# Performance work log

Measured on AMD Instinct MI355X. Metric: run time of the kernel, lower is better.

## Reference

```python
import jax, jax.numpy as jnp
import numpy as np

N_NODES = 100000
N_EDGES = 800000
D_IN = 128
D_HID = 128


def setup_inputs() -> dict:
    key = jax.random.key(0)
    ks = jax.random.split(key, 5)
    x = jax.random.normal(ks[0], (N_NODES, D_IN), dtype=jnp.float32)
    edge_index = jax.random.randint(ks[1], (2, N_EDGES), 0, N_NODES, dtype=jnp.int64)
    W1 = jax.random.normal(ks[2], (D_HID, D_IN), dtype=jnp.float32) * 0.05
    b1 = jnp.zeros((D_HID,), dtype=jnp.float32)
    W2 = jax.random.normal(ks[3], (D_HID, D_HID), dtype=jnp.float32) * 0.05
    b2 = jnp.zeros((D_HID,), dtype=jnp.float32)
    return {"x": x, "edge_index": edge_index, "W1": W1, "b1": b1, "W2": W2, "b2": b2}


def _gcn_conv(x, W, b, src, dst, norm, num_nodes):
    # x' = x @ W^T, then scatter-add normalized messages to dst, then + bias
    h = x @ W.T                                  # [N, d_out]
    msg = h[src] * norm[:, None]                 # [E+N, d_out] gather + scale
    out = jax.ops.segment_sum(msg, dst, num_segments=num_nodes)
    return out + b


def reference(x, edge_index, W1, b1, W2, b2):
    n = x.shape[0]
    loops = jnp.arange(n, dtype=edge_index.dtype)
    src = jnp.concatenate([edge_index[0], loops])  # self-loops appended (PyG GCNConv)
    dst = jnp.concatenate([edge_index[1], loops])
    # symmetric normalization: deg over target nodes (weight 1 per edge)
    deg = jax.ops.segment_sum(jnp.ones_like(dst, dtype=x.dtype), dst, num_segments=n)
    dis = jnp.where(deg > 0, jax.lax.rsqrt(jnp.maximum(deg, 1e-12)), 0.0)
    norm = dis[src] * dis[dst]
    h = jax.nn.relu(_gcn_conv(x, W1, b1, src, dst, norm, n))
    return _gcn_conv(h, W2, b2, src, dst, norm, n)
```

## Files before the change

kernel.cpp:

```cpp
#include <hip/hip_runtime.h>

#define D 128
#define CAP 48
#define BE 4096
#define SC 5120

typedef __attribute__((ext_vector_type(8))) short bf16x8;
typedef __attribute__((ext_vector_type(4))) float f32x4;
typedef __attribute__((ext_vector_type(8))) unsigned short u16x8;

__device__ inline unsigned short f2bf(float f) {
    unsigned u = __float_as_uint(f);
    return (unsigned short)((u + 0x7fff + ((u >> 16) & 1)) >> 16);
}
__device__ inline float bf2f(unsigned short s) {
    return __uint_as_float((unsigned)s << 16);
}
__device__ inline bf16x8 cvt8(const float* __restrict__ p) {
    float4 a = *(const float4*)p;
    float4 b = *(const float4*)(p + 4);
    bf16x8 r;
    r[0] = (short)f2bf(a.x); r[1] = (short)f2bf(a.y);
    r[2] = (short)f2bf(a.z); r[3] = (short)f2bf(a.w);
    r[4] = (short)f2bf(b.x); r[5] = (short)f2bf(b.y);
    r[6] = (short)f2bf(b.z); r[7] = (short)f2bf(b.w);
    return r;
}

__global__ void k_prep(const float* __restrict__ W1, const float* __restrict__ W2,
                       unsigned short* __restrict__ Wb1, unsigned short* __restrict__ Wb2,
                       int* __restrict__ bcnt, int NBK) {
    int i = blockIdx.x * 256 + threadIdx.x;
    if (i < D * D) { Wb1[i] = f2bf(W1[i]); Wb2[i] = f2bf(W2[i]); }
    if (i < NBK) bcnt[i] = 0;
}


template <bool INBF16, bool FOLD>
__device__ inline void gemm_tile(const void* __restrict__ in_v,
                                 const unsigned short* __restrict__ Wb,
                                 const int* __restrict__ cnt,
                                 unsigned short* __restrict__ g,
                                 int N, int tile, int t) {
    int w = t >> 6, l = t & 63;
    int r16 = l & 15, g4 = l >> 4;
    int base = tile * 128 + w * 32;
    int row0 = base + r16, row1 = row0 + 16;
    int cr0 = (row0 < N) ? row0 : N - 1;
    int cr1 = (row1 < N) ? row1 : N - 1;

    f32x4 acc0[8] = {};
    f32x4 acc1[8] = {};
    const unsigned short* wr = Wb + r16 * D + g4 * 8;

#pragma unroll 1
    for (int ks = 0; ks < 4; ks++) {
        bf16x8 b0, b1;
        if (INBF16) {
            const unsigned short* h = (const unsigned short*)in_v;
            b0 = *(const bf16x8*)(h + (size_t)cr0 * D + g4 * 8 + ks * 32);
            b1 = *(const bf16x8*)(h + (size_t)cr1 * D + g4 * 8 + ks * 32);
        } else {
            const float* xx = (const float*)in_v;
            b0 = cvt8(xx + (size_t)cr0 * D + g4 * 8 + ks * 32);
            b1 = cvt8(xx + (size_t)cr1 * D + g4 * 8 + ks * 32);
        }
#pragma unroll
        for (int jt = 0; jt < 8; jt++) {
            bf16x8 a = *(const bf16x8*)(wr + jt * 16 * D + ks * 32);
            acc0[jt] = __builtin_amdgcn_mfma_f32_16x16x32_bf16(a, b0, acc0[jt], 0, 0, 0);
            acc1[jt] = __builtin_amdgcn_mfma_f32_16x16x32_bf16(a, b1, acc1[jt], 0, 0, 0);
        }
    }

#pragma unroll
    for (int tt = 0; tt < 2; tt++) {
        int row = base + tt * 16 + r16;
        if (row < N) {
            float dv = 1.0f;
            if (FOLD) {
                int dg = cnt[row]; if (dg > CAP) dg = CAP;
                dv = rsqrtf((float)(dg + 1));
            }
#pragma unroll
            for (int jt = 0; jt < 8; jt++) {
                f32x4 a = tt ? acc1[jt] : acc0[jt];
                ushort4 o = { f2bf(a[0] * dv), f2bf(a[1] * dv),
                              f2bf(a[2] * dv), f2bf(a[3] * dv) };
                *(ushort4*)&g[(size_t)row * D + jt * 16 + g4 * 4] = o;
            }
        }
    }
}


__global__ __launch_bounds__(256) void k_sort_gemm1(
        const int* __restrict__ ei, int* __restrict__ bcnt, unsigned* __restrict__ brec,
        const float* __restrict__ x, const unsigned short* __restrict__ Wb1,
        unsigned short* __restrict__ g, int N, int E, int ntiles, int fb, int NBK) {
    int bid = blockIdx.x;
    if (bid % 5 == 4) {
        __shared__ unsigned srt[BE];
        __shared__ unsigned char bko[BE];
        __shared__ int hist[256];
        __shared__ int pfx[256];
        __shared__ int gbase[256];
        __shared__ int cur[256];
        int f = bid / 5;
        if (f >= fb) return;
        int t = threadIdx.x;
        int e0 = f * BE;
        int n = E - e0; if (n > BE) n = BE;

        hist[t] = 0; cur[t] = 0;
        __syncthreads();

        unsigned rec[16]; int mb[16];
#pragma unroll
        for (int j = 0; j < 16; j++) {
            int e = e0 + j * 256 + t;
            if (e < E) {
                int s = ei[e], d = ei[E + e];
                rec[j] = ((unsigned)s << 9) | (unsigned)(d & 511);
                mb[j] = d >> 9;
                atomicAdd(&hist[mb[j]], 1);
            } else mb[j] = -1;
        }
        __syncthreads();
        int v = hist[t];
        pfx[t] = v;
        __syncthreads();
        for (int dd = 1; dd < 256; dd <<= 1) {
            int xv = (t >= dd) ? pfx[t - dd] : 0;
            __syncthreads();
            pfx[t] += xv;
            __syncthreads();
        }
        pfx[t] -= v;
        if (v > 0 && t < NBK) gbase[t] = atomicAdd(&bcnt[t], v);
        __syncthreads();
#pragma unroll
        for (int j = 0; j < 16; j++) {
            if (mb[j] >= 0) {
                int p = pfx[mb[j]] + atomicAdd(&cur[mb[j]], 1);
                srt[p] = rec[j];
                bko[p] = (unsigned char)mb[j];
            }
        }
        __syncthreads();
        for (int i = t; i < n; i += 256) {
            int b = bko[i];
            int pos = gbase[b] + (i - pfx[b]);
            if (pos < SC) brec[(size_t)b * SC + pos] = srt[i];
        }
    } else {
        int gid = (bid / 5) * 4 + (bid % 5);
        if (gid >= ntiles) return;
        gemm_tile<false, false>(x, Wb1, nullptr, g, N, gid, threadIdx.x);
    }
}


__global__ __launch_bounds__(256) void k_build(const int* __restrict__ bcnt,
                                               const unsigned* __restrict__ brec,
                                               int* __restrict__ cnt,
                                               int* __restrict__ col, int N) {
    __shared__ int c512[512];
    int b = blockIdx.x, t = threadIdx.x;
    c512[t] = 0; c512[t + 256] = 0;
    __syncthreads();
    int total = bcnt[b]; if (total > SC) total = SC;
    for (int i = t; i < total; i += 256) {
        unsigned rec = brec[(size_t)b * SC + i];
        int dl = rec & 511;
        int p = atomicAdd(&c512[dl], 1);
        if (p < CAP) col[(size_t)(b * 512 + dl) * CAP + p] = (int)(rec >> 9);
    }
    __syncthreads();
#pragma unroll
    for (int k = 0; k < 2; k++) {
        int dl = t + k * 256;
        int node = b * 512 + dl;
        if (node < N) cnt[node] = (c512[dl] < CAP) ? c512[dl] : CAP;
    }
}

__global__ __launch_bounds__(256) void k_gemm2(
        const unsigned short* __restrict__ h, const unsigned short* __restrict__ Wb2,
        const int* __restrict__ cnt, unsigned short* __restrict__ g, int N, int ntiles) {
    if ((int)blockIdx.x >= ntiles) return;
    gemm_tile<true, true>(h, Wb2, cnt, g, N, blockIdx.x, threadIdx.x);
}


template <bool RELU, bool OUT_BF16, bool DISU>
__global__ __launch_bounds__(256) void k_agg(const unsigned short* __restrict__ gtab,
                                             const int* __restrict__ cnt,
                                             const int* __restrict__ col,
                                             const float* __restrict__ bias,
                                             void* __restrict__ out, int N) {
    int node = blockIdx.x * 16 + (threadIdx.x >> 4);
    if (node >= N) return;
    int l16 = threadIdx.x & 15;
    const u16x8* G = (const u16x8*)gtab;
    int deg = cnt[node];
    float disv = rsqrtf((float)(deg + 1));
    float acc[8];
    {
        u16x8 s = G[(size_t)node * 16 + l16];
        float sf = DISU ? disv : 1.0f;
#pragma unroll
        for (int j = 0; j < 8; j++) acc[j] = bf2f(s[j]) * sf;
    }
    const int* cbase = col + (size_t)node * CAP;
    int i = 0;
    for (; i + 3 < deg; i += 4) {
        int u0 = cbase[i], u1 = cbase[i + 1], u2 = cbase[i + 2], u3 = cbase[i + 3];
        u16x8 m0 = G[(size_t)u0 * 16 + l16];
        u16x8 m1 = G[(size_t)u1 * 16 + l16];
        u16x8 m2 = G[(size_t)u2 * 16 + l16];
        u16x8 m3 = G[(size_t)u3 * 16 + l16];
        if (DISU) {
            float d0 = rsqrtf((float)(cnt[u0] + 1));
            float d1 = rsqrtf((float)(cnt[u1] + 1));
            float d2 = rsqrtf((float)(cnt[u2] + 1));
            float d3 = rsqrtf((float)(cnt[u3] + 1));
#pragma unroll
            for (int j = 0; j < 8; j++)
                acc[j] += (bf2f(m0[j]) * d0 + bf2f(m1[j]) * d1)
                        + (bf2f(m2[j]) * d2 + bf2f(m3[j]) * d3);
        } else {
#pragma unroll
            for (int j = 0; j < 8; j++)
                acc[j] += (bf2f(m0[j]) + bf2f(m1[j])) + (bf2f(m2[j]) + bf2f(m3[j]));
        }
    }
    for (; i < deg; i++) {
        int u = cbase[i];
        u16x8 m = G[(size_t)u * 16 + l16];
        float du = DISU ? rsqrtf((float)(cnt[u] + 1)) : 1.0f;
#pragma unroll
        for (int j = 0; j < 8; j++) acc[j] += bf2f(m[j]) * du;
    }
    const float4* B4 = (const float4*)bias;
    float4 bb0 = B4[l16 * 2], bb1 = B4[l16 * 2 + 1];
    float r[8];
    r[0] = fmaf(acc[0], disv, bb0.x); r[1] = fmaf(acc[1], disv, bb0.y);
    r[2] = fmaf(acc[2], disv, bb0.z); r[3] = fmaf(acc[3], disv, bb0.w);
    r[4] = fmaf(acc[4], disv, bb1.x); r[5] = fmaf(acc[5], disv, bb1.y);
    r[6] = fmaf(acc[6], disv, bb1.z); r[7] = fmaf(acc[7], disv, bb1.w);
    if (RELU) {
#pragma unroll
        for (int j = 0; j < 8; j++) r[j] = fmaxf(r[j], 0.f);
    }
    if (OUT_BF16) {
        u16x8 o;
#pragma unroll
        for (int j = 0; j < 8; j++) o[j] = f2bf(r[j]);
        ((u16x8*)out)[(size_t)node * 16 + l16] = o;
    } else {
        float4 o0 = make_float4(r[0], r[1], r[2], r[3]);
        float4 o1 = make_float4(r[4], r[5], r[6], r[7]);
        ((float4*)out)[(size_t)node * 32 + l16 * 2]     = o0;
        ((float4*)out)[(size_t)node * 32 + l16 * 2 + 1] = o1;
    }
}


extern "C" void kernel_launch(void* const* d_in, const int* in_sizes, int n_in,
                              void* d_out, int out_size, void* d_ws, size_t ws_size,
                              hipStream_t stream) {
    const float* x  = (const float*)d_in[0];
    const int*   ei = (const int*)d_in[1];
    const float* W1 = (const float*)d_in[2];
    const float* b1 = (const float*)d_in[3];
    const float* W2 = (const float*)d_in[4];
    const float* b2 = (const float*)d_in[5];
    float* out = (float*)d_out;

    int N = in_sizes[0] / D;
    int E = in_sizes[1] / 2;
    int NBK = (N + 511) >> 9;

    char* w = (char*)d_ws;
    unsigned short* g = (unsigned short*)w;  size_t off = (size_t)N * D * 2;
    off = (off + 255) & ~(size_t)255;
    int* cnt  = (int*)(w + off);             off += (size_t)N * 4;
    off = (off + 255) & ~(size_t)255;
    int* col  = (int*)(w + off);             off += (size_t)NBK * 512 * CAP * 4;
    off = (off + 255) & ~(size_t)255;
    unsigned short* Wb1 = (unsigned short*)(w + off); off += (size_t)D * D * 2;
    unsigned short* Wb2 = (unsigned short*)(w + off); off += (size_t)D * D * 2;
    off = (off + 255) & ~(size_t)255;
    int* bcnt = (int*)(w + off);             off += (size_t)NBK * 4;
    off = (off + 255) & ~(size_t)255;
    unsigned* brec = (unsigned*)(w + off);   off += (size_t)NBK * SC * 4;
    unsigned short* h = (unsigned short*)d_out;

    int ntiles = (N + 127) / 128;
    int fillB  = (E + BE - 1) / BE;
    int fb = fillB > (ntiles + 3) / 4 ? fillB : (ntiles + 3) / 4;
    int total  = 5 * fb;

    k_prep<<<(D * D + 255) / 256, 256, 0, stream>>>(W1, W2, Wb1, Wb2, bcnt, NBK);

    k_sort_gemm1<<<total, 256, 0, stream>>>(ei, bcnt, brec, x, Wb1, g, N, E,
                                            ntiles, fillB, NBK);
    k_build<<<NBK, 256, 0, stream>>>(bcnt, brec, cnt, col, N);

    k_agg<true, true, true><<<(N + 15) / 16, 256, 0, stream>>>(g, cnt, col, b1, h, N);

    k_gemm2<<<ntiles, 256, 0, stream>>>(h, Wb2, cnt, g, N, ntiles);

    k_agg<false, false, false><<<(N + 15) / 16, 256, 0, stream>>>(g, cnt, col, b2, out, N);
}
```

Baseline: 160.1 us.

## Fuse layer-1 aggregation with GEMM2 via LDS and switch to compact CSR

Fuses the first aggregation (with ReLU) and the second GEMM into one kernel. Each block aggregates 128 nodes into an LDS tile and then runs the MFMA GEMM from LDS, so the intermediate h is never written to or read back from global memory. The adjacency changes from fixed-CAP padded rows to an exact CSR built with a per-bucket prefix scan and a global atomic offset, which removes the degree cap and the padding. It also unrolls the gather loops by 8. The cost is an LDS-heavy fused kernel with only 782 blocks, where each 16-lane group handles 8 nodes one after another, which may hurt latency hiding. Bucket order in the CSR becomes nondeterministic.

```diff
diff --git a/kernel.cpp b/kernel.cpp
--- a/kernel.cpp
+++ b/kernel.cpp
@@ -1,9 +1,9 @@
 #include <hip/hip_runtime.h>
 
 #define D 128
-#define CAP 48
 #define BE 4096
 #define SC 5120
+#define LROW 136
 
 typedef __attribute__((ext_vector_type(8))) short bf16x8;
 typedef __attribute__((ext_vector_type(4))) float f32x4;
@@ -29,19 +29,18 @@
 
 __global__ void k_prep(const float* __restrict__ W1, const float* __restrict__ W2,
                        unsigned short* __restrict__ Wb1, unsigned short* __restrict__ Wb2,
-                       int* __restrict__ bcnt, int NBK) {
+                       int* __restrict__ bcnt, int* __restrict__ gcnt, int NBK) {
     int i = blockIdx.x * 256 + threadIdx.x;
     if (i < D * D) { Wb1[i] = f2bf(W1[i]); Wb2[i] = f2bf(W2[i]); }
     if (i < NBK) bcnt[i] = 0;
-}
-
-
-template <bool INBF16, bool FOLD>
-__device__ inline void gemm_tile(const void* __restrict__ in_v,
-                                 const unsigned short* __restrict__ Wb,
-                                 const int* __restrict__ cnt,
-                                 unsigned short* __restrict__ g,
-                                 int N, int tile, int t) {
+    if (i == D * D) *gcnt = 0;
+}
+
+
+__device__ inline void gemm_tile_f32in(const float* __restrict__ xx,
+                                       const unsigned short* __restrict__ Wb,
+                                       unsigned short* __restrict__ g,
+                                       int N, int tile, int t) {
     int w = t >> 6, l = t & 63;
     int r16 = l & 15, g4 = l >> 4;
     int base = tile * 128 + w * 32;
@@ -55,16 +54,8 @@
 
 #pragma unroll 1
     for (int ks = 0; ks < 4; ks++) {
-        bf16x8 b0, b1;
-        if (INBF16) {
-            const unsigned short* h = (const unsigned short*)in_v;
-            b0 = *(const bf16x8*)(h + (size_t)cr0 * D + g4 * 8 + ks * 32);
-            b1 = *(const bf16x8*)(h + (size_t)cr1 * D + g4 * 8 + ks * 32);
-        } else {
-            const float* xx = (const float*)in_v;
-            b0 = cvt8(xx + (size_t)cr0 * D + g4 * 8 + ks * 32);
-            b1 = cvt8(xx + (size_t)cr1 * D + g4 * 8 + ks * 32);
-        }
+        bf16x8 b0 = cvt8(xx + (size_t)cr0 * D + g4 * 8 + ks * 32);
+        bf16x8 b1 = cvt8(xx + (size_t)cr1 * D + g4 * 8 + ks * 32);
 #pragma unroll
         for (int jt = 0; jt < 8; jt++) {
             bf16x8 a = *(const bf16x8*)(wr + jt * 16 * D + ks * 32);
@@ -72,21 +63,14 @@
             acc1[jt] = __builtin_amdgcn_mfma_f32_16x16x32_bf16(a, b1, acc1[jt], 0, 0, 0);
         }
     }
-
 #pragma unroll
     for (int tt = 0; tt < 2; tt++) {
         int row = base + tt * 16 + r16;
         if (row < N) {
-            float dv = 1.0f;
-            if (FOLD) {
-                int dg = cnt[row]; if (dg > CAP) dg = CAP;
-                dv = rsqrtf((float)(dg + 1));
-            }
 #pragma unroll
             for (int jt = 0; jt < 8; jt++) {
                 f32x4 a = tt ? acc1[jt] : acc0[jt];
-                ushort4 o = { f2bf(a[0] * dv), f2bf(a[1] * dv),
-                              f2bf(a[2] * dv), f2bf(a[3] * dv) };
+                ushort4 o = { f2bf(a[0]), f2bf(a[1]), f2bf(a[2]), f2bf(a[3]) };
                 *(ushort4*)&g[(size_t)row * D + jt * 16 + g4 * 4] = o;
             }
         }
@@ -156,7 +140,7 @@
     } else {
         int gid = (bid / 5) * 4 + (bid % 5);
         if (gid >= ntiles) return;
-        gemm_tile<false, false>(x, Wb1, nullptr, g, N, gid, threadIdx.x);
+        gemm_tile_f32in(x, Wb1, g, N, gid, threadIdx.x);
     }
 }
 
@@ -164,106 +148,208 @@
 __global__ __launch_bounds__(256) void k_build(const int* __restrict__ bcnt,
                                                const unsigned* __restrict__ brec,
                                                int* __restrict__ cnt,
-                                               int* __restrict__ col, int N) {
+                                               int* __restrict__ rp,
+                                               int* __restrict__ col,
+                                               int* __restrict__ gcnt, int N) {
     __shared__ int c512[512];
+    __shared__ int base512[512];
+    __shared__ int psc[256];
+    __shared__ int bksum;
     int b = blockIdx.x, t = threadIdx.x;
     c512[t] = 0; c512[t + 256] = 0;
     __syncthreads();
     int total = bcnt[b]; if (total > SC) total = SC;
+    for (int i = t; i < total; i += 256)
+        atomicAdd(&c512[brec[(size_t)b * SC + i] & 511], 1);
+    __syncthreads();
+    int d0 = c512[2 * t], d1 = c512[2 * t + 1];
+    int pair = d0 + d1;
+    psc[t] = pair;
+    __syncthreads();
+    for (int dd = 1; dd < 256; dd <<= 1) {
+        int xv = (t >= dd) ? psc[t - dd] : 0;
+        __syncthreads();
+        psc[t] += xv;
+        __syncthreads();
+    }
+    int pexc = psc[t] - pair;
+    if (t == 255) bksum = atomicAdd(gcnt, psc[255]);
+    __syncthreads();
+    int gb = bksum;
+    base512[2 * t]     = gb + pexc;
+    base512[2 * t + 1] = gb + pexc + d0;
+    c512[2 * t] = 0; c512[2 * t + 1] = 0;
+    __syncthreads();
     for (int i = t; i < total; i += 256) {
         unsigned rec = brec[(size_t)b * SC + i];
         int dl = rec & 511;
         int p = atomicAdd(&c512[dl], 1);
-        if (p < CAP) col[(size_t)(b * 512 + dl) * CAP + p] = (int)(rec >> 9);
+        col[base512[dl] + p] = (int)(rec >> 9);
     }
     __syncthreads();
 #pragma unroll
     for (int k = 0; k < 2; k++) {
         int dl = t + k * 256;
         int node = b * 512 + dl;
-        if (node < N) cnt[node] = (c512[dl] < CAP) ? c512[dl] : CAP;
-    }
-}
-
-__global__ __launch_bounds__(256) void k_gemm2(
-        const unsigned short* __restrict__ h, const unsigned short* __restrict__ Wb2,
-        const int* __restrict__ cnt, unsigned short* __restrict__ g, int N, int ntiles) {
-    if ((int)blockIdx.x >= ntiles) return;
-    gemm_tile<true, true>(h, Wb2, cnt, g, N, blockIdx.x, threadIdx.x);
-}
-
-
-template <bool RELU, bool OUT_BF16, bool DISU>
-__global__ __launch_bounds__(256) void k_agg(const unsigned short* __restrict__ gtab,
-                                             const int* __restrict__ cnt,
-                                             const int* __restrict__ col,
-                                             const float* __restrict__ bias,
-                                             void* __restrict__ out, int N) {
+        if (node < N) { cnt[node] = c512[dl]; rp[node] = base512[dl]; }
+    }
+}
+
+
+__global__ __launch_bounds__(256) void k_agg1_gemm2(
+        const unsigned short* __restrict__ g, const int* __restrict__ cnt,
+        const int* __restrict__ rp, const int* __restrict__ col,
+        const float* __restrict__ b1, const unsigned short* __restrict__ Wb2,
+        unsigned short* __restrict__ g2, int N, int ntiles) {
+    __shared__ __align__(16) unsigned short hl[128 * LROW];
+    int tile = blockIdx.x;
+    if (tile >= ntiles) return;
+    int t = threadIdx.x, grp = t >> 4, l16 = t & 15;
+    const u16x8* G = (const u16x8*)g;
+    const float4* B4 = (const float4*)b1;
+    float4 bb0 = B4[l16 * 2], bb1 = B4[l16 * 2 + 1];
+
+#pragma unroll 1
+    for (int ii = 0; ii < 8; ii++) {
+        int local = grp * 8 + ii;
+        int node = tile * 128 + local;
+        u16x8 hv = {};
+        if (node < N) {
+            int deg = cnt[node];
+            float disv = rsqrtf((float)(deg + 1));
+            float acc[8];
+            u16x8 s = G[(size_t)node * 16 + l16];
+#pragma unroll
+            for (int j = 0; j < 8; j++) acc[j] = bf2f(s[j]) * disv;
+            const int* cb = col + rp[node];
+            int i = 0;
+            for (; i + 7 < deg; i += 8) {
+                int u[8]; u16x8 m[8]; float dd[8];
+#pragma unroll
+                for (int k = 0; k < 8; k++) u[k] = cb[i + k];
+#pragma unroll
+                for (int k = 0; k < 8; k++) m[k] = G[(size_t)u[k] * 16 + l16];
+#pragma unroll
+                for (int k = 0; k < 8; k++) dd[k] = rsqrtf((float)(cnt[u[k]] + 1));
+#pragma unroll
+                for (int j = 0; j < 8; j++) {
+                    float s0 = fmaf(bf2f(m[0][j]), dd[0], bf2f(m[1][j]) * dd[1]);
+                    float s1 = fmaf(bf2f(m[2][j]), dd[2], bf2f(m[3][j]) * dd[3]);
+                    float s2 = fmaf(bf2f(m[4][j]), dd[4], bf2f(m[5][j]) * dd[5]);
+                    float s3 = fmaf(bf2f(m[6][j]), dd[6], bf2f(m[7][j]) * dd[7]);
+                    acc[j] += (s0 + s1) + (s2 + s3);
+                }
+            }
+            for (; i < deg; i++) {
+                int u = cb[i];
+                u16x8 m = G[(size_t)u * 16 + l16];
+                float du = rsqrtf((float)(cnt[u] + 1));
+#pragma unroll
+                for (int j = 0; j < 8; j++) acc[j] += bf2f(m[j]) * du;
+            }
+            float r[8];
+            r[0] = fmaf(acc[0], disv, bb0.x); r[1] = fmaf(acc[1], disv, bb0.y);
+            r[2] = fmaf(acc[2], disv, bb0.z); r[3] = fmaf(acc[3], disv, bb0.w);
+            r[4] = fmaf(acc[4], disv, bb1.x); r[5] = fmaf(acc[5], disv, bb1.y);
+            r[6] = fmaf(acc[6], disv, bb1.z); r[7] = fmaf(acc[7], disv, bb1.w);
+#pragma unroll
+            for (int j = 0; j < 8; j++) hv[j] = f2bf(fmaxf(r[j], 0.f));
+        }
+        *(u16x8*)&hl[local * LROW + l16 * 8] = hv;
+    }
+    __syncthreads();
+
+    int w = t >> 6, l = t & 63;
+    int r16 = l & 15, g4 = l >> 4;
+    int base = tile * 128 + w * 32;
+    f32x4 acc0[8] = {};
+    f32x4 acc1[8] = {};
+    const unsigned short* wr = Wb2 + r16 * D + g4 * 8;
+    int xb0 = (w * 32 + r16) * LROW + g4 * 8;
+    int xb1 = xb0 + 16 * LROW;
+#pragma unroll 1
+    for (int ks = 0; ks < 4; ks++) {
+        bf16x8 b0 = *(const bf16x8*)&hl[xb0 + ks * 32];
+        bf16x8 b1v = *(const bf16x8*)&hl[xb1 + ks * 32];
+#pragma unroll
+        for (int jt = 0; jt < 8; jt++) {
+            bf16x8 a = *(const bf16x8*)(wr + jt * 16 * D + ks * 32);
+            acc0[jt] = __builtin_amdgcn_mfma_f32_16x16x32_bf16(a, b0, acc0[jt], 0, 0, 0);
+            acc1[jt] = __builtin_amdgcn_mfma_f32_16x16x32_bf16(a, b1v, acc1[jt], 0, 0, 0);
+        }
+    }
+#pragma unroll
+    for (int tt = 0; tt < 2; tt++) {
+        int row = base + tt * 16 + r16;
+        if (row < N) {
+            float dv = rsqrtf((float)(cnt[row] + 1));
+#pragma unroll
+            for (int jt = 0; jt < 8; jt++) {
+                f32x4 a = tt ? acc1[jt] : acc0[jt];
+                ushort4 o = { f2bf(a[0] * dv), f2bf(a[1] * dv),
+                              f2bf(a[2] * dv), f2bf(a[3] * dv) };
+                *(ushort4*)&g2[(size_t)row * D + jt * 16 + g4 * 4] = o;
+            }
+        }
+    }
+}
+
+
+__global__ __launch_bounds__(256) void k_agg2(
+        const unsigned short* __restrict__ g2, const int* __restrict__ cnt,
+        const int* __restrict__ rp, const int* __restrict__ col,
+        const float* __restrict__ b2, float* __restrict__ out, int N) {
     int node = blockIdx.x * 16 + (threadIdx.x >> 4);
     if (node >= N) return;
     int l16 = threadIdx.x & 15;
-    const u16x8* G = (const u16x8*)gtab;
-    int deg = cnt[node];
-    float disv = rsqrtf((float)(deg + 1));
+    const u16x8* G = (const u16x8*)g2;
     float acc[8];
     {
         u16x8 s = G[(size_t)node * 16 + l16];
-        float sf = DISU ? disv : 1.0f;
-#pragma unroll
-        for (int j = 0; j < 8; j++) acc[j] = bf2f(s[j]) * sf;
-    }
-    const int* cbase = col + (size_t)node * CAP;
+#pragma unroll
+        for (int j = 0; j < 8; j++) acc[j] = bf2f(s[j]);
+    }
+    int deg = cnt[node];
+    const int* cb = col + rp[node];
     int i = 0;
+    for (; i + 7 < deg; i += 8) {
+        int u[8]; u16x8 m[8];
+#pragma unroll
+        for (int k = 0; k < 8; k++) u[k] = cb[i + k];
+#pragma unroll
+        for (int k = 0; k < 8; k++) m[k] = G[(size_t)u[k] * 16 + l16];
+#pragma unroll
+        for (int j = 0; j < 8; j++) {
+            float s0 = (bf2f(m[0][j]) + bf2f(m[1][j])) + (bf2f(m[2][j]) + bf2f(m[3][j]));
+            float s1 = (bf2f(m[4][j]) + bf2f(m[5][j])) + (bf2f(m[6][j]) + bf2f(m[7][j]));
+            acc[j] += s0 + s1;
+        }
+    }
     for (; i + 3 < deg; i += 4) {
-        int u0 = cbase[i], u1 = cbase[i + 1], u2 = cbase[i + 2], u3 = cbase[i + 3];
+        int u0 = cb[i], u1 = cb[i + 1], u2 = cb[i + 2], u3 = cb[i + 3];
         u16x8 m0 = G[(size_t)u0 * 16 + l16];
         u16x8 m1 = G[(size_t)u1 * 16 + l16];
         u16x8 m2 = G[(size_t)u2 * 16 + l16];
         u16x8 m3 = G[(size_t)u3 * 16 + l16];
-        if (DISU) {
-            float d0 = rsqrtf((float)(cnt[u0] + 1));
-            float d1 = rsqrtf((float)(cnt[u1] + 1));
-            float d2 = rsqrtf((float)(cnt[u2] + 1));
-            float d3 = rsqrtf((float)(cnt[u3] + 1));
-#pragma unroll
-            for (int j = 0; j < 8; j++)
-                acc[j] += (bf2f(m0[j]) * d0 + bf2f(m1[j]) * d1)
-                        + (bf2f(m2[j]) * d2 + bf2f(m3[j]) * d3);
-        } else {
-#pragma unroll
-            for (int j = 0; j < 8; j++)
-                acc[j] += (bf2f(m0[j]) + bf2f(m1[j])) + (bf2f(m2[j]) + bf2f(m3[j]));
-        }
+#pragma unroll
+        for (int j = 0; j < 8; j++)
+            acc[j] += (bf2f(m0[j]) + bf2f(m1[j])) + (bf2f(m2[j]) + bf2f(m3[j]));
     }
     for (; i < deg; i++) {
-        int u = cbase[i];
-        u16x8 m = G[(size_t)u * 16 + l16];
-        float du = DISU ? rsqrtf((float)(cnt[u] + 1)) : 1.0f;
-#pragma unroll
-        for (int j = 0; j < 8; j++) acc[j] += bf2f(m[j]) * du;
-    }
-    const float4* B4 = (const float4*)bias;
+        u16x8 m = G[(size_t)cb[i] * 16 + l16];
+#pragma unroll
+        for (int j = 0; j < 8; j++) acc[j] += bf2f(m[j]);
+    }
+    float disv = rsqrtf((float)(deg + 1));
+    const float4* B4 = (const float4*)b2;
     float4 bb0 = B4[l16 * 2], bb1 = B4[l16 * 2 + 1];
-    float r[8];
-    r[0] = fmaf(acc[0], disv, bb0.x); r[1] = fmaf(acc[1], disv, bb0.y);
-    r[2] = fmaf(acc[2], disv, bb0.z); r[3] = fmaf(acc[3], disv, bb0.w);
-    r[4] = fmaf(acc[4], disv, bb1.x); r[5] = fmaf(acc[5], disv, bb1.y);
-    r[6] = fmaf(acc[6], disv, bb1.z); r[7] = fmaf(acc[7], disv, bb1.w);
-    if (RELU) {
-#pragma unroll
-        for (int j = 0; j < 8; j++) r[j] = fmaxf(r[j], 0.f);
-    }
-    if (OUT_BF16) {
-        u16x8 o;
-#pragma unroll
-        for (int j = 0; j < 8; j++) o[j] = f2bf(r[j]);
-        ((u16x8*)out)[(size_t)node * 16 + l16] = o;
-    } else {
-        float4 o0 = make_float4(r[0], r[1], r[2], r[3]);
-        float4 o1 = make_float4(r[4], r[5], r[6], r[7]);
-        ((float4*)out)[(size_t)node * 32 + l16 * 2]     = o0;
-        ((float4*)out)[(size_t)node * 32 + l16 * 2 + 1] = o1;
-    }
+    float4 o0, o1;
+    o0.x = fmaf(acc[0], disv, bb0.x); o0.y = fmaf(acc[1], disv, bb0.y);
+    o0.z = fmaf(acc[2], disv, bb0.z); o0.w = fmaf(acc[3], disv, bb0.w);
+    o1.x = fmaf(acc[4], disv, bb1.x); o1.y = fmaf(acc[5], disv, bb1.y);
+    o1.z = fmaf(acc[6], disv, bb1.z); o1.w = fmaf(acc[7], disv, bb1.w);
+    ((float4*)out)[(size_t)node * 32 + l16 * 2]     = o0;
+    ((float4*)out)[(size_t)node * 32 + l16 * 2 + 1] = o1;
 }
 
 
@@ -283,34 +369,36 @@
     int NBK = (N + 511) >> 9;
 
     char* w = (char*)d_ws;
-    unsigned short* g = (unsigned short*)w;  size_t off = (size_t)N * D * 2;
+    unsigned short* g  = (unsigned short*)w;  size_t off = (size_t)N * D * 2;
+    off = (off + 255) & ~(size_t)255;
+    unsigned short* g2 = (unsigned short*)(w + off); off += (size_t)N * D * 2;
     off = (off + 255) & ~(size_t)255;
     int* cnt  = (int*)(w + off);             off += (size_t)N * 4;
     off = (off + 255) & ~(size_t)255;
-    int* col  = (int*)(w + off);             off += (size_t)NBK * 512 * CAP * 4;
+    int* rp   = (int*)(w + off);             off += (size_t)N * 4;
+    off = (off + 255) & ~(size_t)255;
+    int* col  = (int*)(w + off);             off += (size_t)E * 4;
     off = (off + 255) & ~(size_t)255;
     unsigned short* Wb1 = (unsigned short*)(w + off); off += (size_t)D * D * 2;
     unsigned short* Wb2 = (unsigned short*)(w + off); off += (size_t)D * D * 2;
     off = (off + 255) & ~(size_t)255;
     int* bcnt = (int*)(w + off);             off += (size_t)NBK * 4;
     off = (off + 255) & ~(size_t)255;
+    int* gcnt = (int*)(w + off);             off += 256;
     unsigned* brec = (unsigned*)(w + off);   off += (size_t)NBK * SC * 4;
-    unsigned short* h = (unsigned short*)d_out;
 
     int ntiles = (N + 127) / 128;
     int fillB  = (E + BE - 1) / BE;
     int fb = fillB > (ntiles + 3) / 4 ? fillB : (ntiles + 3) / 4;
     int total  = 5 * fb;
 
-    k_prep<<<(D * D + 255) / 256, 256, 0, stream>>>(W1, W2, Wb1, Wb2, bcnt, NBK);
+    k_prep<<<(D * D + 511) / 256, 256, 0, stream>>>(W1, W2, Wb1, Wb2, bcnt, gcnt, NBK);
 
     k_sort_gemm1<<<total, 256, 0, stream>>>(ei, bcnt, brec, x, Wb1, g, N, E,
                                             ntiles, fillB, NBK);
-    k_build<<<NBK, 256, 0, stream>>>(bcnt, brec, cnt, col, N);
-
-    k_agg<true, true, true><<<(N + 15) / 16, 256, 0, stream>>>(g, cnt, col, b1, h, N);
-
-    k_gemm2<<<ntiles, 256, 0, stream>>>(h, Wb2, cnt, g, N, ntiles);
-
-    k_agg<false, false, false><<<(N + 15) / 16, 256, 0, stream>>>(g, cnt, col, b2, out, N);
-}
+    k_build<<<NBK, 256, 0, stream>>>(bcnt, brec, cnt, rp, col, gcnt, N);
+
+    k_agg1_gemm2<<<ntiles, 256, 0, stream>>>(g, cnt, rp, col, b1, Wb2, g2, N, ntiles);
+
+    k_agg2<<<(N + 15) / 16, 256, 0, stream>>>(g2, cnt, rp, col, b2, out, N);
+}
```

Measured after the change: 207.8 us. 1.3x slower.

## Replace fixed-capacity adjacency with compact CSR and aggregate two nodes per group

Applied to the files above, without the earlier changes.

Replaces the padded per-node adjacency (capacity 48 slots) with a compact CSR layout: k_build histograms destinations, prefix-sums them, and reserves a global offset per bucket through an atomic counter, then writes columns contiguously. The degree cap is removed, which changes semantics for very high-degree nodes and moves it closer to the reference. Each aggregation thread group now handles two nodes, with masked loads that keep more gathers in flight. A separate g2 buffer is used for the second GEMM output. The CSR build adds a scan and a second pass over the records, and the padded lanes in aggregation issue redundant loads of node n0 (with weight zero) whenever the two degrees differ.

```diff
diff --git a/kernel.cpp b/kernel.cpp
--- a/kernel.cpp
+++ b/kernel.cpp
@@ -1,7 +1,6 @@
 #include <hip/hip_runtime.h>
 
 #define D 128
-#define CAP 48
 #define BE 4096
 #define SC 5120
 
@@ -29,10 +28,11 @@
 
 __global__ void k_prep(const float* __restrict__ W1, const float* __restrict__ W2,
                        unsigned short* __restrict__ Wb1, unsigned short* __restrict__ Wb2,
-                       int* __restrict__ bcnt, int NBK) {
+                       int* __restrict__ bcnt, int* __restrict__ gcnt, int NBK) {
     int i = blockIdx.x * 256 + threadIdx.x;
     if (i < D * D) { Wb1[i] = f2bf(W1[i]); Wb2[i] = f2bf(W2[i]); }
     if (i < NBK) bcnt[i] = 0;
+    if (i == D * D) *gcnt = 0;
 }
 
 
@@ -72,16 +72,12 @@
             acc1[jt] = __builtin_amdgcn_mfma_f32_16x16x32_bf16(a, b1, acc1[jt], 0, 0, 0);
         }
     }
-
 #pragma unroll
     for (int tt = 0; tt < 2; tt++) {
         int row = base + tt * 16 + r16;
         if (row < N) {
             float dv = 1.0f;
-            if (FOLD) {
-                int dg = cnt[row]; if (dg > CAP) dg = CAP;
-                dv = rsqrtf((float)(dg + 1));
-            }
+            if (FOLD) dv = rsqrtf((float)(cnt[row] + 1));
 #pragma unroll
             for (int jt = 0; jt < 8; jt++) {
                 f32x4 a = tt ? acc1[jt] : acc0[jt];
@@ -160,109 +156,178 @@
     }
 }
 
-
 __global__ __launch_bounds__(256) void k_build(const int* __restrict__ bcnt,
                                                const unsigned* __restrict__ brec,
                                                int* __restrict__ cnt,
-                                               int* __restrict__ col, int N) {
+                                               int* __restrict__ rp,
+                                               int* __restrict__ col,
+                                               int* __restrict__ gcnt, int N) {
     __shared__ int c512[512];
+    __shared__ int base512[512];
+    __shared__ int psc[256];
+    __shared__ int bksum;
     int b = blockIdx.x, t = threadIdx.x;
     c512[t] = 0; c512[t + 256] = 0;
     __syncthreads();
     int total = bcnt[b]; if (total > SC) total = SC;
+    for (int i = t; i < total; i += 256)
+        atomicAdd(&c512[brec[(size_t)b * SC + i] & 511], 1);
+    __syncthreads();
+    int d0 = c512[2 * t], d1 = c512[2 * t + 1];
+    int pair = d0 + d1;
+    psc[t] = pair;
+    __syncthreads();
+    for (int dd = 1; dd < 256; dd <<= 1) {
+        int xv = (t >= dd) ? psc[t - dd] : 0;
+        __syncthreads();
+        psc[t] += xv;
+        __syncthreads();
+    }
+    int pexc = psc[t] - pair;
+    if (t == 255) bksum = atomicAdd(gcnt, psc[255]);
+    __syncthreads();
+    int gb = bksum;
+    base512[2 * t]     = gb + pexc;
+    base512[2 * t + 1] = gb + pexc + d0;
+    c512[2 * t] = 0; c512[2 * t + 1] = 0;
+    __syncthreads();
     for (int i = t; i < total; i += 256) {
         unsigned rec = brec[(size_t)b * SC + i];
         int dl = rec & 511;
         int p = atomicAdd(&c512[dl], 1);
-        if (p < CAP) col[(size_t)(b * 512 + dl) * CAP + p] = (int)(rec >> 9);
+        col[base512[dl] + p] = (int)(rec >> 9);
     }
     __syncthreads();
 #pragma unroll
     for (int k = 0; k < 2; k++) {
         int dl = t + k * 256;
         int node = b * 512 + dl;
-        if (node < N) cnt[node] = (c512[dl] < CAP) ? c512[dl] : CAP;
+        if (node < N) { cnt[node] = c512[dl]; rp[node] = base512[dl]; }
     }
 }
 
 __global__ __launch_bounds__(256) void k_gemm2(
         const unsigned short* __restrict__ h, const unsigned short* __restrict__ Wb2,
-        const int* __restrict__ cnt, unsigned short* __restrict__ g, int N, int ntiles) {
+        const int* __restrict__ cnt, unsigned short* __restrict__ g2, int N, int ntiles) {
     if ((int)blockIdx.x >= ntiles) return;
-    gemm_tile<true, true>(h, Wb2, cnt, g, N, blockIdx.x, threadIdx.x);
+    gemm_tile<true, true>(h, Wb2, cnt, g2, N, blockIdx.x, threadIdx.x);
 }
 
 
 template <bool RELU, bool OUT_BF16, bool DISU>
-__global__ __launch_bounds__(256) void k_agg(const unsigned short* __restrict__ gtab,
-                                             const int* __restrict__ cnt,
-                                             const int* __restrict__ col,
-                                             const float* __restrict__ bias,
-                                             void* __restrict__ out, int N) {
-    int node = blockIdx.x * 16 + (threadIdx.x >> 4);
-    if (node >= N) return;
-    int l16 = threadIdx.x & 15;
+__global__ __launch_bounds__(256) void k_agg(
+        const unsigned short* __restrict__ gtab, const int* __restrict__ cnt,
+        const int* __restrict__ rp, const int* __restrict__ col,
+        const float* __restrict__ bias, void* __restrict__ out, int N) {
+    int grp = threadIdx.x >> 4, l16 = threadIdx.x & 15;
+    int n0 = (blockIdx.x * 16 + grp) * 2;
+    if (n0 >= N) return;
+    int n1 = n0 + 1;
+    bool has1 = (n1 < N);
     const u16x8* G = (const u16x8*)gtab;
-    int deg = cnt[node];
-    float disv = rsqrtf((float)(deg + 1));
-    float acc[8];
+
+    int d0 = cnt[n0];
+    int d1 = has1 ? cnt[n1] : 0;
+    float dv0 = rsqrtf((float)(d0 + 1));
+    float dv1 = rsqrtf((float)(d1 + 1));
+    const int* cb0 = col + rp[n0];
+    const int* cb1 = col + (has1 ? rp[n1] : rp[n0]);
+
+    float acc0[8], acc1[8];
     {
-        u16x8 s = G[(size_t)node * 16 + l16];
-        float sf = DISU ? disv : 1.0f;
-#pragma unroll
-        for (int j = 0; j < 8; j++) acc[j] = bf2f(s[j]) * sf;
-    }
-    const int* cbase = col + (size_t)node * CAP;
+        u16x8 s0 = G[(size_t)n0 * 16 + l16];
+        u16x8 s1 = G[(size_t)(has1 ? n1 : n0) * 16 + l16];
+        float f0 = DISU ? dv0 : 1.0f, f1 = DISU ? dv1 : 1.0f;
+#pragma unroll
+        for (int j = 0; j < 8; j++) {
+            acc0[j] = bf2f(s0[j]) * f0;
+            acc1[j] = bf2f(s1[j]) * f1;
+        }
+    }
+    if (!has1) {
+#pragma unroll
+        for (int j = 0; j < 8; j++) acc1[j] = 0.f;
+    }
+
+    int dm = d0 > d1 ? d0 : d1;
     int i = 0;
-    for (; i + 3 < deg; i += 4) {
-        int u0 = cbase[i], u1 = cbase[i + 1], u2 = cbase[i + 2], u3 = cbase[i + 3];
-        u16x8 m0 = G[(size_t)u0 * 16 + l16];
-        u16x8 m1 = G[(size_t)u1 * 16 + l16];
-        u16x8 m2 = G[(size_t)u2 * 16 + l16];
-        u16x8 m3 = G[(size_t)u3 * 16 + l16];
+    for (; i + 3 < dm; i += 4) {
+        int u0[4], u1[4]; float w0[4], w1[4];
+#pragma unroll
+        for (int k = 0; k < 4; k++) {
+            bool v0 = (i + k < d0), v1 = (i + k < d1);
+            u0[k] = v0 ? cb0[i + k] : n0;
+            u1[k] = v1 ? cb1[i + k] : n0;
+            w0[k] = v0 ? 1.0f : 0.0f;
+            w1[k] = v1 ? 1.0f : 0.0f;
+        }
+        u16x8 m0[4], m1[4];
+#pragma unroll
+        for (int k = 0; k < 4; k++) m0[k] = G[(size_t)u0[k] * 16 + l16];
+#pragma unroll
+        for (int k = 0; k < 4; k++) m1[k] = G[(size_t)u1[k] * 16 + l16];
         if (DISU) {
-            float d0 = rsqrtf((float)(cnt[u0] + 1));
-            float d1 = rsqrtf((float)(cnt[u1] + 1));
-            float d2 = rsqrtf((float)(cnt[u2] + 1));
-            float d3 = rsqrtf((float)(cnt[u3] + 1));
-#pragma unroll
-            for (int j = 0; j < 8; j++)
-                acc[j] += (bf2f(m0[j]) * d0 + bf2f(m1[j]) * d1)
-                        + (bf2f(m2[j]) * d2 + bf2f(m3[j]) * d3);
-        } else {
-#pragma unroll
-            for (int j = 0; j < 8; j++)
-                acc[j] += (bf2f(m0[j]) + bf2f(m1[j])) + (bf2f(m2[j]) + bf2f(m3[j]));
-        }
-    }
-    for (; i < deg; i++) {
-        int u = cbase[i];
-        u16x8 m = G[(size_t)u * 16 + l16];
-        float du = DISU ? rsqrtf((float)(cnt[u] + 1)) : 1.0f;
-#pragma unroll
-        for (int j = 0; j < 8; j++) acc[j] += bf2f(m[j]) * du;
-    }
+#pragma unroll
+            for (int k = 0; k < 4; k++) {
+                w0[k] *= rsqrtf((float)(cnt[u0[k]] + 1));
+                w1[k] *= rsqrtf((float)(cnt[u1[k]] + 1));
+            }
+        }
+#pragma unroll
+        for (int j = 0; j < 8; j++) {
+            float a0 = fmaf(bf2f(m0[0][j]), w0[0], bf2f(m0[1][j]) * w0[1]);
+            float b0 = fmaf(bf2f(m0[2][j]), w0[2], bf2f(m0[3][j]) * w0[3]);
+            acc0[j] += a0 + b0;
+            float a1 = fmaf(bf2f(m1[0][j]), w1[0], bf2f(m1[1][j]) * w1[1]);
+            float b1v = fmaf(bf2f(m1[2][j]), w1[2], bf2f(m1[3][j]) * w1[3]);
+            acc1[j] += a1 + b1v;
+        }
+    }
+    for (; i < dm; i++) {
+        if (i < d0) {
+            int u = cb0[i];
+            u16x8 m = G[(size_t)u * 16 + l16];
+            float du = DISU ? rsqrtf((float)(cnt[u] + 1)) : 1.0f;
+#pragma unroll
+            for (int j = 0; j < 8; j++) acc0[j] += bf2f(m[j]) * du;
+        }
+        if (i < d1) {
+            int u = cb1[i];
+            u16x8 m = G[(size_t)u * 16 + l16];
+            float du = DISU ? rsqrtf((float)(cnt[u] + 1)) : 1.0f;
+#pragma unroll
+            for (int j = 0; j < 8; j++) acc1[j] += bf2f(m[j]) * du;
+        }
+    }
+
     const float4* B4 = (const float4*)bias;
     float4 bb0 = B4[l16 * 2], bb1 = B4[l16 * 2 + 1];
-    float r[8];
-    r[0] = fmaf(acc[0], disv, bb0.x); r[1] = fmaf(acc[1], disv, bb0.y);
-    r[2] = fmaf(acc[2], disv, bb0.z); r[3] = fmaf(acc[3], disv, bb0.w);
-    r[4] = fmaf(acc[4], disv, bb1.x); r[5] = fmaf(acc[5], disv, bb1.y);
-    r[6] = fmaf(acc[6], disv, bb1.z); r[7] = fmaf(acc[7], disv, bb1.w);
-    if (RELU) {
-#pragma unroll
-        for (int j = 0; j < 8; j++) r[j] = fmaxf(r[j], 0.f);
-    }
-    if (OUT_BF16) {
-        u16x8 o;
-#pragma unroll
-        for (int j = 0; j < 8; j++) o[j] = f2bf(r[j]);
-        ((u16x8*)out)[(size_t)node * 16 + l16] = o;
-    } else {
-        float4 o0 = make_float4(r[0], r[1], r[2], r[3]);
-        float4 o1 = make_float4(r[4], r[5], r[6], r[7]);
-        ((float4*)out)[(size_t)node * 32 + l16 * 2]     = o0;
-        ((float4*)out)[(size_t)node * 32 + l16 * 2 + 1] = o1;
+#pragma unroll
+    for (int nn = 0; nn < 2; nn++) {
+        if (nn == 1 && !has1) break;
+        int node = nn ? n1 : n0;
+        float dv = nn ? dv1 : dv0;
+        float* ac = nn ? acc1 : acc0;
+        float r[8];
+        r[0] = fmaf(ac[0], dv, bb0.x); r[1] = fmaf(ac[1], dv, bb0.y);
+        r[2] = fmaf(ac[2], dv, bb0.z); r[3] = fmaf(ac[3], dv, bb0.w);
+        r[4] = fmaf(ac[4], dv, bb1.x); r[5] = fmaf(ac[5], dv, bb1.y);
+        r[6] = fmaf(ac[6], dv, bb1.z); r[7] = fmaf(ac[7], dv, bb1.w);
+        if (RELU) {
+#pragma unroll
+            for (int j = 0; j < 8; j++) r[j] = fmaxf(r[j], 0.f);
+        }
+        if (OUT_BF16) {
+            u16x8 o;
+#pragma unroll
+            for (int j = 0; j < 8; j++) o[j] = f2bf(r[j]);
+            ((u16x8*)out)[(size_t)node * 16 + l16] = o;
+        } else {
+            float4 o0 = make_float4(r[0], r[1], r[2], r[3]);
+            float4 o1 = make_float4(r[4], r[5], r[6], r[7]);
+            ((float4*)out)[(size_t)node * 32 + l16 * 2]     = o0;
+            ((float4*)out)[(size_t)node * 32 + l16 * 2 + 1] = o1;
+        }
     }
 }
 
@@ -283,17 +348,22 @@
     int NBK = (N + 511) >> 9;
 
     char* w = (char*)d_ws;
-    unsigned short* g = (unsigned short*)w;  size_t off = (size_t)N * D * 2;
+    unsigned short* g  = (unsigned short*)w;  size_t off = (size_t)N * D * 2;
+    off = (off + 255) & ~(size_t)255;
+    unsigned short* g2 = (unsigned short*)(w + off); off += (size_t)N * D * 2;
     off = (off + 255) & ~(size_t)255;
     int* cnt  = (int*)(w + off);             off += (size_t)N * 4;
     off = (off + 255) & ~(size_t)255;
-    int* col  = (int*)(w + off);             off += (size_t)NBK * 512 * CAP * 4;
+    int* rp   = (int*)(w + off);             off += (size_t)N * 4;
+    off = (off + 255) & ~(size_t)255;
+    int* col  = (int*)(w + off);             off += (size_t)E * 4;
     off = (off + 255) & ~(size_t)255;
     unsigned short* Wb1 = (unsigned short*)(w + off); off += (size_t)D * D * 2;
     unsigned short* Wb2 = (unsigned short*)(w + off); off += (size_t)D * D * 2;
     off = (off + 255) & ~(size_t)255;
     int* bcnt = (int*)(w + off);             off += (size_t)NBK * 4;
     off = (off + 255) & ~(size_t)255;
+    int* gcnt = (int*)(w + off);             off += 256;
     unsigned* brec = (unsigned*)(w + off);   off += (size_t)NBK * SC * 4;
     unsigned short* h = (unsigned short*)d_out;
 
@@ -301,16 +371,17 @@
     int fillB  = (E + BE - 1) / BE;
     int fb = fillB > (ntiles + 3) / 4 ? fillB : (ntiles + 3) / 4;
     int total  = 5 * fb;
-
-    k_prep<<<(D * D + 255) / 256, 256, 0, stream>>>(W1, W2, Wb1, Wb2, bcnt, NBK);
+    int agg_grid = (N + 31) / 32;
+
+    k_prep<<<(D * D + 511) / 256, 256, 0, stream>>>(W1, W2, Wb1, Wb2, bcnt, gcnt, NBK);
 
     k_sort_gemm1<<<total, 256, 0, stream>>>(ei, bcnt, brec, x, Wb1, g, N, E,
                                             ntiles, fillB, NBK);
-    k_build<<<NBK, 256, 0, stream>>>(bcnt, brec, cnt, col, N);
-
-    k_agg<true, true, true><<<(N + 15) / 16, 256, 0, stream>>>(g, cnt, col, b1, h, N);
-
-    k_gemm2<<<ntiles, 256, 0, stream>>>(h, Wb2, cnt, g, N, ntiles);
-
-    k_agg<false, false, false><<<(N + 15) / 16, 256, 0, stream>>>(g, cnt, col, b2, out, N);
-}
+    k_build<<<NBK, 256, 0, stream>>>(bcnt, brec, cnt, rp, col, gcnt, N);
+
+    k_agg<true, true, true><<<agg_grid, 256, 0, stream>>>(g, cnt, rp, col, b1, h, N);
+
+    k_gemm2<<<ntiles, 256, 0, stream>>>(h, Wb2, cnt, g2, N, ntiles);
+
+    k_agg<false, false, false><<<agg_grid, 256, 0, stream>>>(g2, cnt, rp, col, b2, out, N);
+}
```

After: 174.2 us. 8.8% more time.

## Replace capped per-node adjacency with compact CSR and fuse build into gemm1

Applied to the files above, without the earlier changes.

The fixed CAP=48 slots per node are replaced by a compact CSR built with per-bucket prefix scans and a global atomic offset, so col holds exactly E entries and a row-pointer array is added. The CSR build now shares a launch with the first GEMM, while the bucket sort becomes its own kernel that runs first. The second GEMM writes to a separate buffer g2. This drops the degree cap (correctness) and shrinks the col footprint, but adds an extra scan pass and an rp load per node in aggregation.

```diff
diff --git a/kernel.cpp b/kernel.cpp
--- a/kernel.cpp
+++ b/kernel.cpp
@@ -1,7 +1,6 @@
 #include <hip/hip_runtime.h>
 
 #define D 128
-#define CAP 48
 #define BE 4096
 #define SC 5120
 
@@ -29,10 +28,11 @@
 
 __global__ void k_prep(const float* __restrict__ W1, const float* __restrict__ W2,
                        unsigned short* __restrict__ Wb1, unsigned short* __restrict__ Wb2,
-                       int* __restrict__ bcnt, int NBK) {
+                       int* __restrict__ bcnt, int* __restrict__ gcnt, int NBK) {
     int i = blockIdx.x * 256 + threadIdx.x;
     if (i < D * D) { Wb1[i] = f2bf(W1[i]); Wb2[i] = f2bf(W2[i]); }
     if (i < NBK) bcnt[i] = 0;
+    if (i == D * D) *gcnt = 0;
 }
 
 
@@ -72,16 +72,12 @@
             acc1[jt] = __builtin_amdgcn_mfma_f32_16x16x32_bf16(a, b1, acc1[jt], 0, 0, 0);
         }
     }
-
 #pragma unroll
     for (int tt = 0; tt < 2; tt++) {
         int row = base + tt * 16 + r16;
         if (row < N) {
             float dv = 1.0f;
-            if (FOLD) {
-                int dg = cnt[row]; if (dg > CAP) dg = CAP;
-                dv = rsqrtf((float)(dg + 1));
-            }
+            if (FOLD) dv = rsqrtf((float)(cnt[row] + 1));
 #pragma unroll
             for (int jt = 0; jt < 8; jt++) {
                 f32x4 a = tt ? acc1[jt] : acc0[jt];
@@ -94,64 +90,113 @@
 }
 
 
-__global__ __launch_bounds__(256) void k_sort_gemm1(
+__global__ __launch_bounds__(256) void k_sort(
         const int* __restrict__ ei, int* __restrict__ bcnt, unsigned* __restrict__ brec,
+        int E, int NBK) {
+    __shared__ unsigned srt[BE];
+    __shared__ unsigned char bko[BE];
+    __shared__ int hist[256];
+    __shared__ int pfx[256];
+    __shared__ int gbase[256];
+    __shared__ int cur[256];
+    int t = threadIdx.x;
+    int e0 = blockIdx.x * BE;
+    int n = E - e0; if (n > BE) n = BE;
+
+    hist[t] = 0; cur[t] = 0;
+    __syncthreads();
+
+    unsigned rec[16]; int mb[16];
+#pragma unroll
+    for (int j = 0; j < 16; j++) {
+        int e = e0 + j * 256 + t;
+        if (e < E) {
+            int s = ei[e], d = ei[E + e];
+            rec[j] = ((unsigned)s << 9) | (unsigned)(d & 511);
+            mb[j] = d >> 9;
+            atomicAdd(&hist[mb[j]], 1);
+        } else mb[j] = -1;
+    }
+    __syncthreads();
+    int v = hist[t];
+    pfx[t] = v;
+    __syncthreads();
+    for (int dd = 1; dd < 256; dd <<= 1) {
+        int xv = (t >= dd) ? pfx[t - dd] : 0;
+        __syncthreads();
+        pfx[t] += xv;
+        __syncthreads();
+    }
+    pfx[t] -= v;
+    if (v > 0 && t < NBK) gbase[t] = atomicAdd(&bcnt[t], v);
+    __syncthreads();
+#pragma unroll
+    for (int j = 0; j < 16; j++) {
+        if (mb[j] >= 0) {
+            int p = pfx[mb[j]] + atomicAdd(&cur[mb[j]], 1);
+            srt[p] = rec[j];
+            bko[p] = (unsigned char)mb[j];
+        }
+    }
+    __syncthreads();
+    for (int i = t; i < n; i += 256) {
+        int b = bko[i];
+        int pos = gbase[b] + (i - pfx[b]);
+        if (pos < SC) brec[(size_t)b * SC + pos] = srt[i];
+    }
+}
+
+
+__global__ __launch_bounds__(256) void k_build_gemm1(
+        const int* __restrict__ bcnt, const unsigned* __restrict__ brec,
+        int* __restrict__ cnt, int* __restrict__ rp, int* __restrict__ col,
+        int* __restrict__ gcnt,
         const float* __restrict__ x, const unsigned short* __restrict__ Wb1,
-        unsigned short* __restrict__ g, int N, int E, int ntiles, int fb, int NBK) {
+        unsigned short* __restrict__ g, int N, int ntiles, int NBK) {
     int bid = blockIdx.x;
     if (bid % 5 == 4) {
-        __shared__ unsigned srt[BE];
-        __shared__ unsigned char bko[BE];
-        __shared__ int hist[256];
-        __shared__ int pfx[256];
-        __shared__ int gbase[256];
-        __shared__ int cur[256];
-        int f = bid / 5;
-        if (f >= fb) return;
-        int t = threadIdx.x;
-        int e0 = f * BE;
-        int n = E - e0; if (n > BE) n = BE;
-
-        hist[t] = 0; cur[t] = 0;
-        __syncthreads();
-
-        unsigned rec[16]; int mb[16];
-#pragma unroll
-        for (int j = 0; j < 16; j++) {
-            int e = e0 + j * 256 + t;
-            if (e < E) {
-                int s = ei[e], d = ei[E + e];
-                rec[j] = ((unsigned)s << 9) | (unsigned)(d & 511);
-                mb[j] = d >> 9;
-                atomicAdd(&hist[mb[j]], 1);
-            } else mb[j] = -1;
-        }
-        __syncthreads();
-        int v = hist[t];
-        pfx[t] = v;
+        __shared__ int c512[512];
+        __shared__ int base512[512];
+        __shared__ int psc[256];
+        __shared__ int bksum;
+        int b = bid / 5, t = threadIdx.x;
+        if (b >= NBK) return;
+        c512[t] = 0; c512[t + 256] = 0;
+        __syncthreads();
+        int total = bcnt[b]; if (total > SC) total = SC;
+        for (int i = t; i < total; i += 256)
+            atomicAdd(&c512[brec[(size_t)b * SC + i] & 511], 1);
+        __syncthreads();
+        int d0 = c512[2 * t], d1 = c512[2 * t + 1];
+        int pair = d0 + d1;
+        psc[t] = pair;
         __syncthreads();
         for (int dd = 1; dd < 256; dd <<= 1) {
-            int xv = (t >= dd) ? pfx[t - dd] : 0;
+            int xv = (t >= dd) ? psc[t - dd] : 0;
             __syncthreads();
-            pfx[t] += xv;
+            psc[t] += xv;
             __syncthreads();
         }
-        pfx[t] -= v;
-        if (v > 0 && t < NBK) gbase[t] = atomicAdd(&bcnt[t], v);
-        __syncthreads();
-#pragma unroll
-        for (int j = 0; j < 16; j++) {
-            if (mb[j] >= 0) {
-                int p = pfx[mb[j]] + atomicAdd(&cur[mb[j]], 1);
-                srt[p] = rec[j];
-                bko[p] = (unsigned char)mb[j];
-            }
-        }
-        __syncthreads();
-        for (int i = t; i < n; i += 256) {
-            int b = bko[i];
-            int pos = gbase[b] + (i - pfx[b]);
-            if (pos < SC) brec[(size_t)b * SC + pos] = srt[i];
+        int pexc = psc[t] - pair;
+        if (t == 255) bksum = atomicAdd(gcnt, psc[255]);
+        __syncthreads();
+        int gb = bksum;
+        base512[2 * t]     = gb + pexc;
+        base512[2 * t + 1] = gb + pexc + d0;
+        c512[2 * t] = 0; c512[2 * t + 1] = 0;
+        __syncthreads();
+        for (int i = t; i < total; i += 256) {
+            unsigned rec = brec[(size_t)b * SC + i];
+            int dl = rec & 511;
+            int p = atomicAdd(&c512[dl], 1);
+            col[base512[dl] + p] = (int)(rec >> 9);
+        }
+        __syncthreads();
+#pragma unroll
+        for (int k = 0; k < 2; k++) {
+            int dl = t + k * 256;
+            int node = b * 512 + dl;
+            if (node < N) { cnt[node] = c512[dl]; rp[node] = base512[dl]; }
         }
     } else {
         int gid = (bid / 5) * 4 + (bid % 5);
@@ -160,45 +205,19 @@
     }
 }
 
-
-__global__ __launch_bounds__(256) void k_build(const int* __restrict__ bcnt,
-                                               const unsigned* __restrict__ brec,
-                                               int* __restrict__ cnt,
-                                               int* __restrict__ col, int N) {
-    __shared__ int c512[512];
-    int b = blockIdx.x, t = threadIdx.x;
-    c512[t] = 0; c512[t + 256] = 0;
-    __syncthreads();
-    int total = bcnt[b]; if (total > SC) total = SC;
-    for (int i = t; i < total; i += 256) {
-        unsigned rec = brec[(size_t)b * SC + i];
-        int dl = rec & 511;
-        int p = atomicAdd(&c512[dl], 1);
-        if (p < CAP) col[(size_t)(b * 512 + dl) * CAP + p] = (int)(rec >> 9);
-    }
-    __syncthreads();
-#pragma unroll
-    for (int k = 0; k < 2; k++) {
-        int dl = t + k * 256;
-        int node = b * 512 + dl;
-        if (node < N) cnt[node] = (c512[dl] < CAP) ? c512[dl] : CAP;
-    }
-}
-
 __global__ __launch_bounds__(256) void k_gemm2(
         const unsigned short* __restrict__ h, const unsigned short* __restrict__ Wb2,
-        const int* __restrict__ cnt, unsigned short* __restrict__ g, int N, int ntiles) {
+        const int* __restrict__ cnt, unsigned short* __restrict__ g2, int N, int ntiles) {
     if ((int)blockIdx.x >= ntiles) return;
-    gemm_tile<true, true>(h, Wb2, cnt, g, N, blockIdx.x, threadIdx.x);
+    gemm_tile<true, true>(h, Wb2, cnt, g2, N, blockIdx.x, threadIdx.x);
 }
 
 
 template <bool RELU, bool OUT_BF16, bool DISU>
-__global__ __launch_bounds__(256) void k_agg(const unsigned short* __restrict__ gtab,
-                                             const int* __restrict__ cnt,
-                                             const int* __restrict__ col,
-                                             const float* __restrict__ bias,
-                                             void* __restrict__ out, int N) {
+__global__ __launch_bounds__(256) void k_agg(
+        const unsigned short* __restrict__ gtab, const int* __restrict__ cnt,
+        const int* __restrict__ rp, const int* __restrict__ col,
+        const float* __restrict__ bias, void* __restrict__ out, int N) {
     int node = blockIdx.x * 16 + (threadIdx.x >> 4);
     if (node >= N) return;
     int l16 = threadIdx.x & 15;
@@ -212,10 +231,10 @@
 #pragma unroll
         for (int j = 0; j < 8; j++) acc[j] = bf2f(s[j]) * sf;
     }
-    const int* cbase = col + (size_t)node * CAP;
+    const int* cb = col + rp[node];
     int i = 0;
     for (; i + 3 < deg; i += 4) {
-        int u0 = cbase[i], u1 = cbase[i + 1], u2 = cbase[i + 2], u3 = cbase[i + 3];
+        int u0 = cb[i], u1 = cb[i + 1], u2 = cb[i + 2], u3 = cb[i + 3];
         u16x8 m0 = G[(size_t)u0 * 16 + l16];
         u16x8 m1 = G[(size_t)u1 * 16 + l16];
         u16x8 m2 = G[(size_t)u2 * 16 + l16];
@@ -236,7 +255,7 @@
         }
     }
     for (; i < deg; i++) {
-        int u = cbase[i];
+        int u = cb[i];
         u16x8 m = G[(size_t)u * 16 + l16];
         float du = DISU ? rsqrtf((float)(cnt[u] + 1)) : 1.0f;
 #pragma unroll
@@ -283,34 +302,41 @@
     int NBK = (N + 511) >> 9;
 
     char* w = (char*)d_ws;
-    unsigned short* g = (unsigned short*)w;  size_t off = (size_t)N * D * 2;
+    unsigned short* g  = (unsigned short*)w;  size_t off = (size_t)N * D * 2;
+    off = (off + 255) & ~(size_t)255;
+    unsigned short* g2 = (unsigned short*)(w + off); off += (size_t)N * D * 2;
     off = (off + 255) & ~(size_t)255;
     int* cnt  = (int*)(w + off);             off += (size_t)N * 4;
     off = (off + 255) & ~(size_t)255;
-    int* col  = (int*)(w + off);             off += (size_t)NBK * 512 * CAP * 4;
+    int* rp   = (int*)(w + off);             off += (size_t)N * 4;
+    off = (off + 255) & ~(size_t)255;
+    int* col  = (int*)(w + off);             off += (size_t)E * 4;
     off = (off + 255) & ~(size_t)255;
     unsigned short* Wb1 = (unsigned short*)(w + off); off += (size_t)D * D * 2;
     unsigned short* Wb2 = (unsigned short*)(w + off); off += (size_t)D * D * 2;
     off = (off + 255) & ~(size_t)255;
     int* bcnt = (int*)(w + off);             off += (size_t)NBK * 4;
     off = (off + 255) & ~(size_t)255;
+    int* gcnt = (int*)(w + off);             off += 256;
     unsigned* brec = (unsigned*)(w + off);   off += (size_t)NBK * SC * 4;
     unsigned short* h = (unsigned short*)d_out;
 
     int ntiles = (N + 127) / 128;
-    int fillB  = (E + BE - 1) / BE;
-    int fb = fillB > (ntiles + 3) / 4 ? fillB : (ntiles + 3) / 4;
+    int sortB  = (E + BE - 1) / BE;
+    int fb = NBK > (ntiles + 3) / 4 ? NBK : (ntiles + 3) / 4;
     int total  = 5 * fb;
-
-    k_prep<<<(D * D + 255) / 256, 256, 0, stream>>>(W1, W2, Wb1, Wb2, bcnt, NBK);
-
-    k_sort_gemm1<<<total, 256, 0, stream>>>(ei, bcnt, brec, x, Wb1, g, N, E,
-                                            ntiles, fillB, NBK);
-    k_build<<<NBK, 256, 0, stream>>>(bcnt, brec, cnt, col, N);
-
-    k_agg<true, true, true><<<(N + 15) / 16, 256, 0, stream>>>(g, cnt, col, b1, h, N);
-
-    k_gemm2<<<ntiles, 256, 0, stream>>>(h, Wb2, cnt, g, N, ntiles);
-
-    k_agg<false, false, false><<<(N + 15) / 16, 256, 0, stream>>>(g, cnt, col, b2, out, N);
-}
+    int agg_grid = (N + 15) / 16;
+
+    k_prep<<<(D * D + 511) / 256, 256, 0, stream>>>(W1, W2, Wb1, Wb2, bcnt, gcnt, NBK);
+
+    k_sort<<<sortB, 256, 0, stream>>>(ei, bcnt, brec, E, NBK);
+
+    k_build_gemm1<<<total, 256, 0, stream>>>(bcnt, brec, cnt, rp, col, gcnt,
+                                             x, Wb1, g, N, ntiles, NBK);
+
+    k_agg<true, true, true><<<agg_grid, 256, 0, stream>>>(g, cnt, rp, col, b1, h, N);
+
+    k_gemm2<<<ntiles, 256, 0, stream>>>(h, Wb2, cnt, g2, N, ntiles);
+
+    k_agg<false, false, false><<<agg_grid, 256, 0, stream>>>(g2, cnt, rp, col, b2, out, N);
+}
```

After: 161.6 us. No clear change (+1.0%).
